# Kernel optimization log

Measured on AMD Instinct MI355X. Metric: run time of the kernel, lower is better.

## Reference

```python
import jax, jax.numpy as jnp
import numpy as np

C = 128   # in_channels
K = 7     # local attention kernel_size
B, H, W = 1, 128, 128
PAD = K // 2


def conv_bn(x, w, s, b, relu=True):
    # 1x1 conv (no bias) + folded eval-mode BatchNorm (per-channel scale/bias)
    y = jnp.einsum('bchw,oc->bohw', x, w)
    y = y * s[None, :, None, None] + b[None, :, None, None]
    return jax.nn.relu(y) if relu else y


def local_attention(q, k, v, ksize):
    # q,k,v: (B,C,H,W). Windowed self-attention over ksize x ksize neighborhood
    # (equivalent to F.unfold(key/value, ksize, padding=ksize//2) + dot + softmax + weighted sum)
    pad = ksize // 2
    kp = jnp.pad(k, ((0, 0), (0, 0), (pad, pad), (pad, pad)))
    vp = jnp.pad(v, ((0, 0), (0, 0), (pad, pad), (pad, pad)))
    Hh, Ww = q.shape[2], q.shape[3]
    offsets = [(i, j) for i in range(ksize) for j in range(ksize)]
    # sim: (B, k*k, H, W) -- dot over channels per window offset
    sim = jnp.stack([jnp.einsum('bchw,bchw->bhw', q, kp[:, :, i:i + Hh, j:j + Ww])
                     for (i, j) in offsets], axis=1)
    attn = jax.nn.softmax(sim, axis=1)
    out = jnp.zeros_like(q)
    for idx, (i, j) in enumerate(offsets):
        out = out + attn[:, idx][:, None] * vp[:, :, i:i + Hh, j:j + Ww]
    return out


def setup_inputs() -> dict:
    key = jax.random.key(0)
    ks = jax.random.split(key, 19)
    d = {'x': jax.random.normal(ks[0], (B, C, H, W), jnp.float32)}
    names = ['q1', 'q2', 'k1', 'k2', 'v', 'o']
    for idx, n in enumerate(names):
        cin = 2 * C if n == 'o' else C
        kw, ksc, kb = ks[1 + 3 * idx], ks[2 + 3 * idx], ks[3 + 3 * idx]
        d['w_' + n] = jax.random.normal(kw, (C, cin), jnp.float32) / np.sqrt(cin).astype(np.float32)
        d['s_' + n] = jax.random.uniform(ksc, (C,), jnp.float32, 0.5, 1.5)
        d['b_' + n] = jax.random.normal(kb, (C,), jnp.float32) * 0.1
    return d


def reference(x, w_q1, s_q1, b_q1, w_q2, s_q2, b_q2,
              w_k1, s_k1, b_k1, w_k2, s_k2, b_k2,
              w_v, s_v, b_v, w_o, s_o, b_o):
    # query/key projections: two ConvBNReLU 1x1; value: one ConvBNReLU 1x1
    q = conv_bn(conv_bn(x, w_q1, s_q1, b_q1), w_q2, s_q2, b_q2)
    k = conv_bn(conv_bn(x, w_k1, s_k1, b_k1), w_k2, s_k2, b_k2)
    v = conv_bn(x, w_v, s_v, b_v)
    new_feat = local_attention(q, k, v, K)
    # integration: cat([attn_out, x], dim=1) -> 1x1 conv + BN (no activation)
    cat = jnp.concatenate([new_feat, x], axis=1)  # (B, 2C, H, W)
    return conv_bn(cat, w_o, s_o, b_o, relu=False)
```

## Files before the change

kernel.cpp:

```cpp
#include <hip/hip_runtime.h>


typedef short short8 __attribute__((ext_vector_type(8)));
typedef short short4v __attribute__((ext_vector_type(4)));
typedef float f32x4 __attribute__((ext_vector_type(4)));

#define HW_PIX 16384
#define CH 128
#define PADW 134
#define PSLOT (134 * 134 * 128)

#define WQ1_OFF 0
#define WQ2_OFF 16384
#define WK1_OFF 32768
#define WK2_OFF 49152
#define WV_OFF  65536
#define WO_OFF  81920
#define SB_OFF  114688
#define TQ_OFF  117760
#define XT_OFF  (TQ_OFF + 2097152)
#define KP_OFF  (XT_OFF + 2097152)
#define VP_OFF  (KP_OFF + PSLOT)

static __device__ __forceinline__ float bf2f(unsigned short u) {
    union { unsigned int i; float f; } c; c.i = ((unsigned int)u) << 16; return c.f;
}
static __device__ __forceinline__ unsigned short f2bf(float f) {
    union { unsigned int i; float f; } c; c.f = f;
    unsigned int x = c.i;
    return (unsigned short)((x + 0x7fffu + ((x >> 16) & 1u)) >> 16);
}

struct CvtArgs { const float* w[6]; const float* sb[12]; };

__global__ __launch_bounds__(256)
void cvt_k(CvtArgs a, short* __restrict__ ws)
{
    const int u = blockIdx.x * 256 + threadIdx.x;
    if (u < 14336) {
        const int s0 = u * 8;
        const int seg = (s0 < 81920) ? (s0 >> 14) : 5;
        const int base = (seg < 5) ? (seg << 14) : 81920;
        const float* fp = a.w[seg] + (s0 - base);
        short8 o;
        #pragma unroll
        for (int j = 0; j < 8; ++j) o[j] = (short)f2bf(fp[j]);
        *(short8*)(ws + s0) = o;
    } else if (u < 15872) {
        const int idx = u - 14336;
        ((float*)(ws + SB_OFF))[idx] = a.sb[idx >> 7][idx & 127];
    } else if (u < 15872 + 3144) {
        const int idx = u - 15872;
        const int buf = idx / 1572;
        const int e   = idx % 1572;
        int row, col;
        if (e < 402)      { row = e / PADW;          col = e % PADW; }
        else if (e < 804) { row = 131 + (e - 402) / PADW; col = (e - 402) % PADW; }
        else { const int r = e - 804; row = 3 + r / 6; const int c = r % 6;
               col = (c < 3) ? c : (128 + c); }
        short* p = ws + (buf ? VP_OFF : KP_OFF) + (row * PADW + col) * CH;
        const short8 z = {0, 0, 0, 0, 0, 0, 0, 0};
        #pragma unroll
        for (int j = 0; j < 16; ++j) *(short8*)(p + j * 8) = z;
    }
}

__global__ __launch_bounds__(256)
void qkv_k(const float* __restrict__ x, short* __restrict__ ws)
{
    const float* sb = (const float*)(ws + SB_OFF);
    const int tid = threadIdx.x;
    const int bid = blockIdx.x;
    const int t   = (bid & 7) * 128 + (bid >> 3);
    const int tr = t >> 5, tc = t & 31;
    const int h0 = tr * 4, w0 = tc * 4;

    const int l16 = tid & 15;
    const int g   = (tid & 63) >> 4;
    const int wv  = tid >> 6;
    const int o0  = wv * 32;

    __shared__ short xb[16 * 136];
    __shared__ short tileQ[16 * 136];
    __shared__ short tileK[16 * 136];
    __shared__ short tileV[16 * 136];

    #pragma unroll
    for (int pass = 0; pass < 2; ++pass) {
        const int u = tid + pass * 256;
        const int c = u >> 2, r = u & 3;
        f32x4 v = *(const f32x4*)(x + c * HW_PIX + (h0 + r) * 128 + w0);
        #pragma unroll
        for (int j = 0; j < 4; ++j) xb[(r * 4 + j) * 136 + c] = (short)f2bf(v[j]);
    }
    __syncthreads();

    {
        const int px = tid >> 4, c8 = tid & 15;
        const int p_img = (h0 + (px >> 2)) * 128 + w0 + (px & 3);
        *(short8*)(ws + XT_OFF + p_img * CH + c8 * 8) =
            *(const short8*)(xb + px * 136 + c8 * 8);
    }

    short8 xa[4];
    #pragma unroll
    for (int kk = 0; kk < 4; ++kk)
        xa[kk] = *(const short8*)(xb + l16 * 136 + kk * 32 + g * 8);

    const f32x4 z = {0.f, 0.f, 0.f, 0.f};
    f32x4 acc[2];

    #define GEMM1(WOFF, SIDX, TILE)                                              \
    {                                                                            \
        acc[0] = z; acc[1] = z;                                                  \
        _Pragma("unroll")                                                        \
        for (int kk = 0; kk < 4; ++kk) {                                         \
            _Pragma("unroll")                                                    \
            for (int nt = 0; nt < 2; ++nt) {                                     \
                short8 bv = *(const short8*)(ws + WOFF +                         \
                    (o0 + nt * 16 + l16) * 128 + kk * 32 + g * 8);               \
                acc[nt] = __builtin_amdgcn_mfma_f32_16x16x32_bf16(xa[kk], bv, acc[nt], 0, 0, 0); \
            }                                                                    \
        }                                                                        \
        _Pragma("unroll")                                                        \
        for (int nt = 0; nt < 2; ++nt) {                                         \
            const int o = o0 + nt * 16 + l16;                                    \
            const float sf = sb[(SIDX) * 128 + o], bf = sb[(SIDX + 1) * 128 + o];\
            _Pragma("unroll")                                                    \
            for (int i = 0; i < 4; ++i) {                                        \
                const float vl = fmaxf(acc[nt][i] * sf + bf, 0.f);               \
                TILE[(g * 4 + i) * 136 + o] = (short)f2bf(vl);                   \
            }                                                                    \
        }                                                                        \
    }
    GEMM1(WQ1_OFF, 0, tileQ)
    GEMM1(WK1_OFF, 4, tileK)
    GEMM1(WV_OFF,  8, tileV)
    #undef GEMM1

    __syncthreads();

    short8 lf[4];
    f32x4 accQ[2], accK[2];
    accQ[0] = z; accQ[1] = z; accK[0] = z; accK[1] = z;
    #pragma unroll
    for (int kk = 0; kk < 4; ++kk) lf[kk] = *(const short8*)(tileQ + l16 * 136 + kk * 32 + g * 8);
    #pragma unroll
    for (int kk = 0; kk < 4; ++kk) {
        #pragma unroll
        for (int nt = 0; nt < 2; ++nt) {
            short8 bv = *(const short8*)(ws + WQ2_OFF + (o0 + nt * 16 + l16) * 128 + kk * 32 + g * 8);
            accQ[nt] = __builtin_amdgcn_mfma_f32_16x16x32_bf16(lf[kk], bv, accQ[nt], 0, 0, 0);
        }
    }
    #pragma unroll
    for (int kk = 0; kk < 4; ++kk) lf[kk] = *(const short8*)(tileK + l16 * 136 + kk * 32 + g * 8);
    #pragma unroll
    for (int kk = 0; kk < 4; ++kk) {
        #pragma unroll
        for (int nt = 0; nt < 2; ++nt) {
            short8 bv = *(const short8*)(ws + WK2_OFF + (o0 + nt * 16 + l16) * 128 + kk * 32 + g * 8);
            accK[nt] = __builtin_amdgcn_mfma_f32_16x16x32_bf16(lf[kk], bv, accK[nt], 0, 0, 0);
        }
    }
    __syncthreads();

    #pragma unroll
    for (int nt = 0; nt < 2; ++nt) {
        const int o = o0 + nt * 16 + l16;
        const float sfq = sb[2 * 128 + o], bfq = sb[3 * 128 + o];
        const float sfk = sb[6 * 128 + o], bfk = sb[7 * 128 + o];
        #pragma unroll
        for (int i = 0; i < 4; ++i) {
            tileQ[(g * 4 + i) * 136 + o] = (short)f2bf(fmaxf(accQ[nt][i] * sfq + bfq, 0.f));
            tileK[(g * 4 + i) * 136 + o] = (short)f2bf(fmaxf(accK[nt][i] * sfk + bfk, 0.f));
        }
    }
    __syncthreads();

    {
        const int px = tid >> 4, c8 = tid & 15;
        const int soff = px * 136 + c8 * 8;
        const int p_img = (h0 + (px >> 2)) * 128 + w0 + (px & 3);
        const int pr = h0 + (px >> 2) + 3, pc = w0 + (px & 3) + 3;
        const int doff = (pr * PADW + pc) * CH + c8 * 8;
        *(short8*)(ws + TQ_OFF + p_img * CH + c8 * 8) = *(const short8*)(tileQ + soff);
        *(short8*)(ws + KP_OFF + doff) = *(const short8*)(tileK + soff);
        *(short8*)(ws + VP_OFF + doff) = *(const short8*)(tileV + soff);
    }
}

__global__ __launch_bounds__(256, 5)
void att_k(const short* __restrict__ ws, float* __restrict__ out)
{
    const float* sb = (const float*)(ws + SB_OFF);

    __shared__ __align__(16) short halKV[100 * 128];
    __shared__ __align__(16) float Pf[16 * 100];

    short* attB = halKV;
    short* outT = halKV + 2176;

    const int tid = threadIdx.x;
    const int bid = blockIdx.x;
    const int t   = (bid & 7) * 128 + (bid >> 3);
    const int tr = t >> 5, tc = t & 31;
    const int h0 = tr * 4, w0 = tc * 4;

    const int l16 = tid & 15;
    const int g   = (tid & 63) >> 4;
    const int wv  = tid >> 6;
    const f32x4 z4 = {0.f, 0.f, 0.f, 0.f};

    const int ap_img = (h0 + (l16 >> 2)) * 128 + w0 + (l16 & 3);

    short8 af[4];
    #pragma unroll
    for (int kk = 0; kk < 4; ++kk)
        af[kk] = *(const short8*)(ws + TQ_OFF + ap_img * CH + kk * 32 + g * 8);

    for (int u = tid; u < 1600; u += 256) {
        const int di = u / 160, rem = u - di * 160;
        const int j = rem >> 4, c8 = rem & 15;
        *(short8*)(halKV + (di * 10 + j) * 128 + c8 * 8) =
            *(const short8*)(ws + KP_OFF + ((h0 + di) * PADW + (w0 + j)) * CH + c8 * 8);
    }
    __syncthreads();

    #pragma unroll
    for (int s = 0; s < 2; ++s) {
        const int nt = wv + s * 4;
        if (nt < 7) {
            f32x4 sa = z4;
            #pragma unroll
            for (int kk = 0; kk < 4; ++kk) {
                short8 bv = *(const short8*)(halKV + (nt * 16 + l16) * 128 + kk * 32 + g * 8);
                sa = __builtin_amdgcn_mfma_f32_16x16x32_bf16(af[kk], bv, sa, 0, 0, 0);
            }
            const int col = nt * 16 + l16;
            if (col < 100) {
                #pragma unroll
                for (int i = 0; i < 4; ++i)
                    Pf[(g * 4 + i) * 100 + col] = sa[i];
            }
        }
    }
    __syncthreads();

    for (int u = tid; u < 1600; u += 256) {
        const int di = u / 160, rem = u - di * 160;
        const int j = rem >> 4, c8 = rem & 15;
        *(short8*)(halKV + (di * 10 + j) * 128 + c8 * 8) =
            *(const short8*)(ws + VP_OFF + ((h0 + di) * PADW + (w0 + j)) * CH + c8 * 8);
    }

    const int px = tid >> 4;
    const int r = px >> 2, cl = px & 3;
    float rz;
    {
        float vals[7];
        float mx = -3.0e38f;
        #pragma unroll
        for (int n = 0; n < 7; ++n) {
            const int hp = n * 16 + l16;
            float v = -3.0e38f;
            if (hp < 100) {
                const int hr = hp / 10, hc = hp - (hp / 10) * 10;
                if ((unsigned)(hr - r) < 7u && (unsigned)(hc - cl) < 7u)
                    v = Pf[px * 100 + hp];
            }
            vals[n] = v; mx = fmaxf(mx, v);
        }
        mx = fmaxf(mx, __shfl_xor(mx, 1, 16));
        mx = fmaxf(mx, __shfl_xor(mx, 2, 16));
        mx = fmaxf(mx, __shfl_xor(mx, 4, 16));
        mx = fmaxf(mx, __shfl_xor(mx, 8, 16));
        float zs = 0.f;
        #pragma unroll
        for (int n = 0; n < 7; ++n) {
            const int hp = n * 16 + l16;
            const float ev = (vals[n] > -1.0e37f) ? __expf(vals[n] - mx) : 0.f;
            zs += ev;
            if (hp < 100) Pf[px * 100 + hp] = ev;
        }
        zs += __shfl_xor(zs, 1, 16);
        zs += __shfl_xor(zs, 2, 16);
        zs += __shfl_xor(zs, 4, 16);
        zs += __shfl_xor(zs, 8, 16);
        rz = 1.0f / zs;
    }
    __syncthreads();

    float of[8];
    {
        const int cb = l16 * 8;
        #pragma unroll
        for (int j = 0; j < 8; ++j) of[j] = 0.f;
        #pragma unroll
        for (int off = 0; off < 49; ++off) {
            const int di = off / 7, dj = off % 7;
            const int hp = (r + di) * 10 + cl + dj;
            const float ev = Pf[px * 100 + hp];
            short8 vv = *(const short8*)(halKV + hp * 128 + cb);
            #pragma unroll
            for (int j = 0; j < 8; ++j) of[j] += ev * bf2f((unsigned short)vv[j]);
        }
    }
    __syncthreads();

    {
        const int cb = l16 * 8;
        short8 ov;
        #pragma unroll
        for (int j = 0; j < 8; ++j) ov[j] = (short)f2bf(of[j] * rz);
        *(short8*)(attB + px * 136 + cb) = ov;
    }
    __syncthreads();

    const int o0 = wv * 32;
    f32x4 fac[2];
    fac[0] = z4; fac[1] = z4;
    #pragma unroll
    for (int kk = 0; kk < 8; ++kk) {
        const int kbase = kk * 32 + g * 8;
        short8 av;
        if (kk < 4) av = *(const short8*)(attB + l16 * 136 + kbase);
        else        av = *(const short8*)(ws + XT_OFF + ap_img * CH + (kbase - 128));
        #pragma unroll
        for (int nt = 0; nt < 2; ++nt) {
            short8 bv = *(const short8*)(ws + WO_OFF + (o0 + nt * 16 + l16) * 256 + kbase);
            fac[nt] = __builtin_amdgcn_mfma_f32_16x16x32_bf16(av, bv, fac[nt], 0, 0, 0);
        }
    }
    {
        const float* s  = sb + 10 * 128;
        const float* bb = sb + 11 * 128;
        #pragma unroll
        for (int nt = 0; nt < 2; ++nt) {
            const int o = o0 + nt * 16 + l16;
            const float sf = s[o], bf = bb[o];
            #pragma unroll
            for (int i = 0; i < 4; ++i)
                outT[o * 24 + g * 4 + i] = (short)f2bf(fac[nt][i] * sf + bf);
        }
    }
    __syncthreads();
    #pragma unroll
    for (int pass = 0; pass < 2; ++pass) {
        const int u = tid + pass * 256;
        const int c = u >> 2, rr = u & 3;
        short4v sv = *(const short4v*)(outT + c * 24 + rr * 4);
        f32x4 fv;
        #pragma unroll
        for (int j = 0; j < 4; ++j) fv[j] = bf2f((unsigned short)sv[j]);
        *(f32x4*)(out + c * HW_PIX + (h0 + rr) * 128 + w0) = fv;
    }
}

extern "C" void kernel_launch(void* const* d_in, const int* in_sizes, int n_in,
                              void* d_out, int out_size, void* d_ws, size_t ws_size,
                              hipStream_t stream)
{
    const float* x = (const float*)d_in[0];
    short* ws = (short*)d_ws;

    CvtArgs ca;
    ca.w[0] = (const float*)d_in[1];
    ca.w[1] = (const float*)d_in[4];
    ca.w[2] = (const float*)d_in[7];
    ca.w[3] = (const float*)d_in[10];
    ca.w[4] = (const float*)d_in[13];
    ca.w[5] = (const float*)d_in[16];
    ca.sb[0]  = (const float*)d_in[2];  ca.sb[1]  = (const float*)d_in[3];
    ca.sb[2]  = (const float*)d_in[5];  ca.sb[3]  = (const float*)d_in[6];
    ca.sb[4]  = (const float*)d_in[8];  ca.sb[5]  = (const float*)d_in[9];
    ca.sb[6]  = (const float*)d_in[11]; ca.sb[7]  = (const float*)d_in[12];
    ca.sb[8]  = (const float*)d_in[14]; ca.sb[9]  = (const float*)d_in[15];
    ca.sb[10] = (const float*)d_in[17]; ca.sb[11] = (const float*)d_in[18];

    cvt_k<<<dim3(75), dim3(256), 0, stream>>>(ca, ws);
    qkv_k<<<dim3(1024), dim3(256), 0, stream>>>(x, ws);
    att_k<<<dim3(1024), dim3(256), 0, stream>>>(ws, (float*)d_out);
}
```

Before: 56.78 us.

## Drop weight-conversion/padding kernel; convert weights inline and mask borders in attention

Removes the separate cvt_k launch that converted weights to bf16, copied scale/bias, and zeroed the padded K/V borders. Weights are now read as fp32 and converted to bf16 on the fly in each GEMM. Out-of-image window positions are handled by explicit masking in the softmax and the V accumulation, so the padding no longer needs zeroing. This saves one kernel launch and its serialization, at the cost of twice the weight load bandwidth and redundant conversions in every block, plus extra branch logic in the attention loop.

```diff
diff --git a/kernel.cpp b/kernel.cpp
--- a/kernel.cpp
+++ b/kernel.cpp
@@ -10,14 +10,7 @@
 #define PADW 134
 #define PSLOT (134 * 134 * 128)
 
-#define WQ1_OFF 0
-#define WQ2_OFF 16384
-#define WK1_OFF 32768
-#define WK2_OFF 49152
-#define WV_OFF  65536
-#define WO_OFF  81920
-#define SB_OFF  114688
-#define TQ_OFF  117760
+#define TQ_OFF  0
 #define XT_OFF  (TQ_OFF + 2097152)
 #define KP_OFF  (XT_OFF + 2097152)
 #define VP_OFF  (KP_OFF + PSLOT)
@@ -31,44 +24,27 @@
     return (unsigned short)((x + 0x7fffu + ((x >> 16) & 1u)) >> 16);
 }
 
-struct CvtArgs { const float* w[6]; const float* sb[12]; };
+static __device__ __forceinline__ short8 ldw8(const float* wp) {
+    f32x4 a = *(const f32x4*)wp;
+    f32x4 b = *(const f32x4*)(wp + 4);
+    short8 o;
+    #pragma unroll
+    for (int j = 0; j < 4; ++j) { o[j] = (short)f2bf(a[j]); o[4 + j] = (short)f2bf(b[j]); }
+    return o;
+}
+
+struct QkvArgs {
+    const float* x;
+    const float* w_q1; const float* s_q1; const float* b_q1;
+    const float* w_q2; const float* s_q2; const float* b_q2;
+    const float* w_k1; const float* s_k1; const float* b_k1;
+    const float* w_k2; const float* s_k2; const float* b_k2;
+    const float* w_v;  const float* s_v;  const float* b_v;
+};
 
 __global__ __launch_bounds__(256)
-void cvt_k(CvtArgs a, short* __restrict__ ws)
+void qkv_k(QkvArgs a, short* __restrict__ ws)
 {
-    const int u = blockIdx.x * 256 + threadIdx.x;
-    if (u < 14336) {
-        const int s0 = u * 8;
-        const int seg = (s0 < 81920) ? (s0 >> 14) : 5;
-        const int base = (seg < 5) ? (seg << 14) : 81920;
-        const float* fp = a.w[seg] + (s0 - base);
-        short8 o;
-        #pragma unroll
-        for (int j = 0; j < 8; ++j) o[j] = (short)f2bf(fp[j]);
-        *(short8*)(ws + s0) = o;
-    } else if (u < 15872) {
-        const int idx = u - 14336;
-        ((float*)(ws + SB_OFF))[idx] = a.sb[idx >> 7][idx & 127];
-    } else if (u < 15872 + 3144) {
-        const int idx = u - 15872;
-        const int buf = idx / 1572;
-        const int e   = idx % 1572;
-        int row, col;
-        if (e < 402)      { row = e / PADW;          col = e % PADW; }
-        else if (e < 804) { row = 131 + (e - 402) / PADW; col = (e - 402) % PADW; }
-        else { const int r = e - 804; row = 3 + r / 6; const int c = r % 6;
-               col = (c < 3) ? c : (128 + c); }
-        short* p = ws + (buf ? VP_OFF : KP_OFF) + (row * PADW + col) * CH;
-        const short8 z = {0, 0, 0, 0, 0, 0, 0, 0};
-        #pragma unroll
-        for (int j = 0; j < 16; ++j) *(short8*)(p + j * 8) = z;
-    }
-}
-
-__global__ __launch_bounds__(256)
-void qkv_k(const float* __restrict__ x, short* __restrict__ ws)
-{
-    const float* sb = (const float*)(ws + SB_OFF);
     const int tid = threadIdx.x;
     const int bid = blockIdx.x;
     const int t   = (bid & 7) * 128 + (bid >> 3);
@@ -89,7 +65,7 @@
     for (int pass = 0; pass < 2; ++pass) {
         const int u = tid + pass * 256;
         const int c = u >> 2, r = u & 3;
-        f32x4 v = *(const f32x4*)(x + c * HW_PIX + (h0 + r) * 128 + w0);
+        f32x4 v = *(const f32x4*)(a.x + c * HW_PIX + (h0 + r) * 128 + w0);
         #pragma unroll
         for (int j = 0; j < 4; ++j) xb[(r * 4 + j) * 136 + c] = (short)f2bf(v[j]);
     }
@@ -110,22 +86,21 @@
     const f32x4 z = {0.f, 0.f, 0.f, 0.f};
     f32x4 acc[2];
 
-    #define GEMM1(WOFF, SIDX, TILE)                                              \
+    #define GEMM1(WPTR, SPTR, BPTR, TILE)                                        \
     {                                                                            \
         acc[0] = z; acc[1] = z;                                                  \
         _Pragma("unroll")                                                        \
         for (int kk = 0; kk < 4; ++kk) {                                         \
             _Pragma("unroll")                                                    \
             for (int nt = 0; nt < 2; ++nt) {                                     \
-                short8 bv = *(const short8*)(ws + WOFF +                         \
-                    (o0 + nt * 16 + l16) * 128 + kk * 32 + g * 8);               \
+                short8 bv = ldw8(WPTR + (o0 + nt * 16 + l16) * 128 + kk * 32 + g * 8); \
                 acc[nt] = __builtin_amdgcn_mfma_f32_16x16x32_bf16(xa[kk], bv, acc[nt], 0, 0, 0); \
             }                                                                    \
         }                                                                        \
         _Pragma("unroll")                                                        \
         for (int nt = 0; nt < 2; ++nt) {                                         \
             const int o = o0 + nt * 16 + l16;                                    \
-            const float sf = sb[(SIDX) * 128 + o], bf = sb[(SIDX + 1) * 128 + o];\
+            const float sf = (SPTR)[o], bf = (BPTR)[o];                          \
             _Pragma("unroll")                                                    \
             for (int i = 0; i < 4; ++i) {                                        \
                 const float vl = fmaxf(acc[nt][i] * sf + bf, 0.f);               \
@@ -133,10 +108,9 @@
             }                                                                    \
         }                                                                        \
     }
-    GEMM1(WQ1_OFF, 0, tileQ)
-    GEMM1(WK1_OFF, 4, tileK)
-    GEMM1(WV_OFF,  8, tileV)
-    #undef GEMM1
+    GEMM1(a.w_q1, a.s_q1, a.b_q1, tileQ)
+    GEMM1(a.w_k1, a.s_k1, a.b_k1, tileK)
+    GEMM1(a.w_v,  a.s_v,  a.b_v,  tileV)
 
     __syncthreads();
 
@@ -149,7 +123,7 @@
     for (int kk = 0; kk < 4; ++kk) {
         #pragma unroll
         for (int nt = 0; nt < 2; ++nt) {
-            short8 bv = *(const short8*)(ws + WQ2_OFF + (o0 + nt * 16 + l16) * 128 + kk * 32 + g * 8);
+            short8 bv = ldw8(a.w_q2 + (o0 + nt * 16 + l16) * 128 + kk * 32 + g * 8);
             accQ[nt] = __builtin_amdgcn_mfma_f32_16x16x32_bf16(lf[kk], bv, accQ[nt], 0, 0, 0);
         }
     }
@@ -159,7 +133,7 @@
     for (int kk = 0; kk < 4; ++kk) {
         #pragma unroll
         for (int nt = 0; nt < 2; ++nt) {
-            short8 bv = *(const short8*)(ws + WK2_OFF + (o0 + nt * 16 + l16) * 128 + kk * 32 + g * 8);
+            short8 bv = ldw8(a.w_k2 + (o0 + nt * 16 + l16) * 128 + kk * 32 + g * 8);
             accK[nt] = __builtin_amdgcn_mfma_f32_16x16x32_bf16(lf[kk], bv, accK[nt], 0, 0, 0);
         }
     }
@@ -168,8 +142,8 @@
     #pragma unroll
     for (int nt = 0; nt < 2; ++nt) {
         const int o = o0 + nt * 16 + l16;
-        const float sfq = sb[2 * 128 + o], bfq = sb[3 * 128 + o];
-        const float sfk = sb[6 * 128 + o], bfk = sb[7 * 128 + o];
+        const float sfq = a.s_q2[o], bfq = a.b_q2[o];
+        const float sfk = a.s_k2[o], bfk = a.b_k2[o];
         #pragma unroll
         for (int i = 0; i < 4; ++i) {
             tileQ[(g * 4 + i) * 136 + o] = (short)f2bf(fmaxf(accQ[nt][i] * sfq + bfq, 0.f));
@@ -188,13 +162,14 @@
         *(short8*)(ws + KP_OFF + doff) = *(const short8*)(tileK + soff);
         *(short8*)(ws + VP_OFF + doff) = *(const short8*)(tileV + soff);
     }
+    #undef GEMM1
 }
 
 __global__ __launch_bounds__(256, 5)
-void att_k(const short* __restrict__ ws, float* __restrict__ out)
+void att_k(const short* __restrict__ ws, const float* __restrict__ wo,
+           const float* __restrict__ so, const float* __restrict__ bo,
+           float* __restrict__ out)
 {
-    const float* sb = (const float*)(ws + SB_OFF);
-
     __shared__ __align__(16) short halKV[100 * 128];
     __shared__ __align__(16) float Pf[16 * 100];
 
@@ -266,8 +241,11 @@
             float v = -3.0e38f;
             if (hp < 100) {
                 const int hr = hp / 10, hc = hp - (hp / 10) * 10;
-                if ((unsigned)(hr - r) < 7u && (unsigned)(hc - cl) < 7u)
-                    v = Pf[px * 100 + hp];
+                if ((unsigned)(hr - r) < 7u && (unsigned)(hc - cl) < 7u) {
+                    const bool in_img = ((unsigned)(h0 + hr - 3) < 128u) &&
+                                        ((unsigned)(w0 + hc - 3) < 128u);
+                    v = in_img ? Pf[px * 100 + hp] : 0.0f;
+                }
             }
             vals[n] = v; mx = fmaxf(mx, v);
         }
@@ -299,11 +277,15 @@
         #pragma unroll
         for (int off = 0; off < 49; ++off) {
             const int di = off / 7, dj = off % 7;
-            const int hp = (r + di) * 10 + cl + dj;
-            const float ev = Pf[px * 100 + hp];
-            short8 vv = *(const short8*)(halKV + hp * 128 + cb);
-            #pragma unroll
-            for (int j = 0; j < 8; ++j) of[j] += ev * bf2f((unsigned short)vv[j]);
+            const bool in_img = ((unsigned)(h0 + r + di - 3) < 128u) &&
+                                ((unsigned)(w0 + cl + dj - 3) < 128u);
+            if (in_img) {
+                const int hp = (r + di) * 10 + cl + dj;
+                const float ev = Pf[px * 100 + hp];
+                short8 vv = *(const short8*)(halKV + hp * 128 + cb);
+                #pragma unroll
+                for (int j = 0; j < 8; ++j) of[j] += ev * bf2f((unsigned short)vv[j]);
+            }
         }
     }
     __syncthreads();
@@ -328,17 +310,15 @@
         else        av = *(const short8*)(ws + XT_OFF + ap_img * CH + (kbase - 128));
         #pragma unroll
         for (int nt = 0; nt < 2; ++nt) {
-            short8 bv = *(const short8*)(ws + WO_OFF + (o0 + nt * 16 + l16) * 256 + kbase);
+            short8 bv = ldw8(wo + (o0 + nt * 16 + l16) * 256 + kbase);
             fac[nt] = __builtin_amdgcn_mfma_f32_16x16x32_bf16(av, bv, fac[nt], 0, 0, 0);
         }
     }
     {
-        const float* s  = sb + 10 * 128;
-        const float* bb = sb + 11 * 128;
         #pragma unroll
         for (int nt = 0; nt < 2; ++nt) {
             const int o = o0 + nt * 16 + l16;
-            const float sf = s[o], bf = bb[o];
+            const float sf = so[o], bf = bo[o];
             #pragma unroll
             for (int i = 0; i < 4; ++i)
                 outT[o * 24 + g * 4 + i] = (short)f2bf(fac[nt][i] * sf + bf);
@@ -361,24 +341,18 @@
                               void* d_out, int out_size, void* d_ws, size_t ws_size,
                               hipStream_t stream)
 {
-    const float* x = (const float*)d_in[0];
     short* ws = (short*)d_ws;
 
-    CvtArgs ca;
-    ca.w[0] = (const float*)d_in[1];
-    ca.w[1] = (const float*)d_in[4];
-    ca.w[2] = (const float*)d_in[7];
-    ca.w[3] = (const float*)d_in[10];
-    ca.w[4] = (const float*)d_in[13];
-    ca.w[5] = (const float*)d_in[16];
-    ca.sb[0]  = (const float*)d_in[2];  ca.sb[1]  = (const float*)d_in[3];
-    ca.sb[2]  = (const float*)d_in[5];  ca.sb[3]  = (const float*)d_in[6];
-    ca.sb[4]  = (const float*)d_in[8];  ca.sb[5]  = (const float*)d_in[9];
-    ca.sb[6]  = (const float*)d_in[11]; ca.sb[7]  = (const float*)d_in[12];
-    ca.sb[8]  = (const float*)d_in[14]; ca.sb[9]  = (const float*)d_in[15];
-    ca.sb[10] = (const float*)d_in[17]; ca.sb[11] = (const float*)d_in[18];
-
-    cvt_k<<<dim3(75), dim3(256), 0, stream>>>(ca, ws);
-    qkv_k<<<dim3(1024), dim3(256), 0, stream>>>(x, ws);
-    att_k<<<dim3(1024), dim3(256), 0, stream>>>(ws, (float*)d_out);
-}
+    QkvArgs qa;
+    qa.x    = (const float*)d_in[0];
+    qa.w_q1 = (const float*)d_in[1];  qa.s_q1 = (const float*)d_in[2];  qa.b_q1 = (const float*)d_in[3];
+    qa.w_q2 = (const float*)d_in[4];  qa.s_q2 = (const float*)d_in[5];  qa.b_q2 = (const float*)d_in[6];
+    qa.w_k1 = (const float*)d_in[7];  qa.s_k1 = (const float*)d_in[8];  qa.b_k1 = (const float*)d_in[9];
+    qa.w_k2 = (const float*)d_in[10]; qa.s_k2 = (const float*)d_in[11]; qa.b_k2 = (const float*)d_in[12];
+    qa.w_v  = (const float*)d_in[13]; qa.s_v  = (const float*)d_in[14]; qa.b_v  = (const float*)d_in[15];
+
+    qkv_k<<<dim3(1024), dim3(256), 0, stream>>>(qa, ws);
+    att_k<<<dim3(1024), dim3(256), 0, stream>>>(
+        ws, (const float*)d_in[16], (const float*)d_in[17], (const float*)d_in[18],
+        (float*)d_out);
+}
```

Measured after the change: 76.93 us. 35.5% more time.
